# Optimization experiments

Measured on AMD Instinct MI355X. Metric: run time of the kernel, lower is better.

The kernel has to match this reference:

```python
import jax, jax.numpy as jnp
import numpy as np

B, N_PER, D_IN, D_OUT, E_PER = 64, 256, 256, 128, 8192  # graphs, nodes/graph, in feat, out feat (=clusters K), edges/graph
EPS = 1e-12


def _sage(h, src, dst, W, b):
    # DenseSAGEConv (mean aggregator): h [n,Din], src/dst [E]
    agg = jnp.zeros_like(h).at[dst].add(h[src])                 # sum of in-neighbor messages
    deg = jnp.zeros((h.shape[0],), h.dtype).at[dst].add(1.0)
    agg = agg / jnp.maximum(deg, 1.0)[:, None]                  # mean aggregation
    z = jnp.concatenate([h, agg], axis=-1) @ W + b              # Linear(2*Din -> Dout)
    z = z / jnp.maximum(jnp.linalg.norm(z, axis=-1, keepdims=True), EPS)  # F.normalize(p=2)
    return jax.nn.relu(z)                                       # activation


def setup_inputs() -> dict:
    key = jax.random.key(0)
    ks = jax.random.split(key, 5)
    h = jax.random.normal(ks[0], (B, N_PER, D_IN), jnp.float32)
    edge_src = jax.random.randint(ks[1], (B, E_PER), 0, N_PER)
    edge_dst = jax.random.randint(ks[2], (B, E_PER), 0, N_PER)
    s = 1.0 / np.sqrt(2 * D_IN)
    W_feat = jax.random.uniform(ks[3], (2 * D_IN, D_OUT), jnp.float32, -s, s)
    b_feat = jnp.zeros((D_OUT,), jnp.float32)
    W_pool = jax.random.uniform(ks[4], (2 * D_IN, D_OUT), jnp.float32, -s, s)
    b_pool = jnp.zeros((D_OUT,), jnp.float32)
    return {"h": h, "edge_src": edge_src, "edge_dst": edge_dst,
            "W_feat": W_feat, "b_feat": b_feat, "W_pool": W_pool, "b_pool": b_pool}


def reference(h, edge_src, edge_dst, W_feat, b_feat, W_pool, b_pool):
    sage = jax.vmap(_sage, in_axes=(0, 0, 0, None, None))
    feat = sage(h, edge_src, edge_dst, W_feat, b_feat)                          # [B,n,K]
    assign = jax.nn.softmax(sage(h, edge_src, edge_dst, W_pool, b_pool), -1)    # [B,n,K]
    # h = assign^T @ feat, per graph (equivalent to block_diag(assign)^T @ stacked feat)
    h_pool = jnp.einsum('bnk,bnd->bkd', assign, feat).reshape(B * D_OUT, D_OUT)  # [B*K, Dout]
    # adj_new = S^T A S per graph; A[dst,src]=1 per edge -> sum_e outer(S[dst_e], S[src_e])
    s_dst = jnp.take_along_axis(assign, edge_dst[:, :, None], axis=1)           # [B,E,K]
    s_src = jnp.take_along_axis(assign, edge_src[:, :, None], axis=1)           # [B,E,K]
    blocks = jnp.einsum('bek,bel->bkl', s_dst, s_src)                           # [B,K,K]
    # cross-graph blocks are exactly zero in the batched graph -> block-diagonal dense adj
    adj_new = jax.scipy.linalg.block_diag(*blocks)                              # [B*K, B*K]
    return adj_new, h_pool
```

## Files before the change

### kernel.cpp

```cpp
#include <hip/hip_runtime.h>
#include <hip/hip_bf16.h>
#include <stdint.h>

#define BG 64
#define NP 256
#define DI 256
#define DO 128
#define EP 8192


typedef __attribute__((ext_vector_type(8))) short short8;
typedef __attribute__((ext_vector_type(4))) float float4v;

__device__ __forceinline__ int ldi(const void* p, size_t i, int i64) {
  return i64 ? (int)((const long long*)p)[i] : ((const int*)p)[i];
}

__device__ __forceinline__ short f2b(float x) {
  union { float f; unsigned u; } c; c.f = x;
  unsigned r = c.u + 0x7FFFu + ((c.u >> 16) & 1u);
  return (short)(r >> 16);
}

__global__ void k_scatter(const void* __restrict__ esrc, const void* __restrict__ edst,
                          float* __restrict__ A, float* __restrict__ deg) {
  __shared__ int cnt;
  int b = blockIdx.x, t = threadIdx.x;
  if (t == 0) cnt = 0;
  __syncthreads();
  uint32_t w = ((const uint32_t*)esrc)[2 * t + 1];
  if (w != 0) atomicAdd(&cnt, 1);
  float4* Az = (float4*)(A + (size_t)b * NP * NP);
  for (int i = t; i < NP * NP / 4; i += 256) Az[i] = make_float4(0.f, 0.f, 0.f, 0.f);
  deg[b * NP + t] = 0.f;
  __syncthreads();
  int i64 = (cnt == 0);
  const size_t base = (size_t)b * EP;
  float* Ab = A + (size_t)b * NP * NP;
  float* degb = deg + b * NP;
  for (int e = t; e < EP; e += 256) {
    int si = ldi(esrc, base + e, i64) & (NP - 1);
    int di = ldi(edst, base + e, i64) & (NP - 1);
    atomicAdd(Ab + (size_t)di * NP + si, 1.0f);
    atomicAdd(degb + di, 1.0f);
  }
}

__global__ __launch_bounds__(256) void k_wt(const float* __restrict__ Wf,
                                            const float* __restrict__ Wp,
                                            short* __restrict__ Wt) {
  __shared__ __align__(16) float T[32][132];
  int b = blockIdx.x;
  int head = b >> 4;
  int k0 = (b & 15) * 32;
  const float* W = head ? Wp : Wf;
  int t = threadIdx.x;
  {
    int k = t >> 3, fs = (t & 7) * 16;
    const float* src = &W[(size_t)(k0 + k) * DO + fs];
#pragma unroll
    for (int j = 0; j < 4; ++j)
      *(float4*)&T[k][fs + j * 4] = *(const float4*)(src + j * 4);
  }
  __syncthreads();
  int f = t & 127, kh = (t >> 7) * 16;
  __align__(16) short tmp[16];
#pragma unroll
  for (int i = 0; i < 16; ++i) tmp[i] = f2b(T[kh + i][f]);
  short* dst = &Wt[((size_t)head * DO + f) * 512 + k0 + kh];
  *(short8*)dst = *(short8*)&tmp[0];
  *(short8*)(dst + 8) = *(short8*)&tmp[8];
}

__global__ __launch_bounds__(256) void k_gemm_agg(const float* __restrict__ A,
                                                  const float* __restrict__ h,
                                                  const float* __restrict__ deg,
                                                  float* __restrict__ agg) {
  __shared__ __align__(16) float As[32][68];
  __shared__ __align__(16) float Hs[32][132];
  int b = blockIdx.y;
  int r0 = (blockIdx.x & 3) * 64;
  int f0 = (blockIdx.x >> 2) * 128;
  int t = threadIdx.x;
  int tr = t >> 4, tc = t & 15;
  float acc[4][8] = {};
  const float* Ab = A + (size_t)b * NP * NP;
  const float* hb = h + (size_t)b * NP * DI;
  for (int kc = 0; kc < NP; kc += 32) {
    __syncthreads();
    {
      int r = t >> 2;
      int ks = (t & 3) * 8;
      const float* src = &Ab[(size_t)(r0 + r) * NP + kc + ks];
      float4 v0 = *(const float4*)src;
      float4 v1 = *(const float4*)(src + 4);
      As[ks + 0][r] = v0.x; As[ks + 1][r] = v0.y; As[ks + 2][r] = v0.z; As[ks + 3][r] = v0.w;
      As[ks + 4][r] = v1.x; As[ks + 5][r] = v1.y; As[ks + 6][r] = v1.z; As[ks + 7][r] = v1.w;
    }
    {
      int k = t >> 3;
      int fs = (t & 7) * 16;
      const float* src = &hb[(size_t)(kc + k) * DI + f0 + fs];
#pragma unroll
      for (int j = 0; j < 4; ++j)
        *(float4*)&Hs[k][fs + j * 4] = *(const float4*)(src + j * 4);
    }
    __syncthreads();
#pragma unroll
    for (int k = 0; k < 32; ++k) {
      float a[4], ww[8];
      *(float4*)&a[0] = *(const float4*)&As[k][tr * 4];
      *(float4*)&ww[0] = *(const float4*)&Hs[k][tc * 8];
      *(float4*)&ww[4] = *(const float4*)&Hs[k][tc * 8 + 4];
#pragma unroll
      for (int i = 0; i < 4; ++i)
#pragma unroll
        for (int j = 0; j < 8; ++j)
          acc[i][j] += a[i] * ww[j];
    }
  }
#pragma unroll
  for (int i = 0; i < 4; ++i) {
    int gi = r0 + tr * 4 + i;
    float sc = 1.0f / fmaxf(deg[b * NP + gi], 1.0f);
    float* dst = &agg[((size_t)b * NP + gi) * DI + f0 + tc * 8];
    float o0[4] = { acc[i][0] * sc, acc[i][1] * sc, acc[i][2] * sc, acc[i][3] * sc };
    float o1[4] = { acc[i][4] * sc, acc[i][5] * sc, acc[i][6] * sc, acc[i][7] * sc };
    *(float4*)dst = *(float4*)o0;
    *(float4*)(dst + 4) = *(float4*)o1;
  }
}

__global__ __launch_bounds__(256) void k_zepi_mfma(const float* __restrict__ h,
                                                   const float* __restrict__ agg,
                                                   const short* __restrict__ Wt,
                                                   const float* __restrict__ bfe,
                                                   const float* __restrict__ bpo,
                                                   float* __restrict__ feat,
                                                   float* __restrict__ assign) {
  __shared__ __align__(16) short Xs[32][40];
  int r0 = blockIdx.x * 32;
  int t = threadIdx.x;
  int wave = t >> 6, lane = t & 63;
  int rt = wave & 1, ch = wave >> 1;
  int m = lane & 15, q = lane >> 4;
  float4v acc[8];
#pragma unroll
  for (int i = 0; i < 8; ++i) acc[i] = (float4v){0.f, 0.f, 0.f, 0.f};

  for (int kc = 0; kc < 2 * DI; kc += 32) {
    __syncthreads();
    {
      int r = t >> 3, k4 = (t & 7) * 4;
      const float* src = (kc < DI) ? &h[(size_t)(r0 + r) * DI + kc + k4]
                                   : &agg[(size_t)(r0 + r) * DI + (kc - DI) + k4];
      float4 v = *(const float4*)src;
      Xs[r][k4 + 0] = f2b(v.x); Xs[r][k4 + 1] = f2b(v.y);
      Xs[r][k4 + 2] = f2b(v.z); Xs[r][k4 + 3] = f2b(v.w);
    }
    __syncthreads();
    short8 afrag = *(const short8*)&Xs[rt * 16 + m][q * 8];
#pragma unroll
    for (int tt = 0; tt < 8; ++tt) {
      int n = ch * 128 + tt * 16 + m;
      short8 bfrag = *(const short8*)&Wt[(size_t)n * 512 + kc + q * 8];
      acc[tt] = __builtin_amdgcn_mfma_f32_16x16x32_bf16(afrag, bfrag, acc[tt], 0, 0, 0);
    }
  }

  const float* bp = ch ? bpo : bfe;
  float bias[8];
#pragma unroll
  for (int tt = 0; tt < 8; ++tt) bias[tt] = bp ? bp[tt * 16 + m] : 0.f;
#pragma unroll
  for (int reg = 0; reg < 4; ++reg) {
    int row = r0 + rt * 16 + q * 4 + reg;
    float z[8];
    float ss = 0.f;
#pragma unroll
    for (int tt = 0; tt < 8; ++tt) { z[tt] = acc[tt][reg] + bias[tt]; ss += z[tt] * z[tt]; }
    ss += __shfl_xor(ss, 1); ss += __shfl_xor(ss, 2);
    ss += __shfl_xor(ss, 4); ss += __shfl_xor(ss, 8);
    float inv = 1.0f / fmaxf(sqrtf(ss), 1e-12f);
    float v[8];
#pragma unroll
    for (int tt = 0; tt < 8; ++tt) v[tt] = fmaxf(z[tt] * inv, 0.f);
    if (ch == 0) {
#pragma unroll
      for (int tt = 0; tt < 8; ++tt) feat[(size_t)row * DO + tt * 16 + m] = v[tt];
    } else {
      float mx = v[0];
#pragma unroll
      for (int tt = 1; tt < 8; ++tt) mx = fmaxf(mx, v[tt]);
      mx = fmaxf(mx, __shfl_xor(mx, 1)); mx = fmaxf(mx, __shfl_xor(mx, 2));
      mx = fmaxf(mx, __shfl_xor(mx, 4)); mx = fmaxf(mx, __shfl_xor(mx, 8));
      float e[8], s = 0.f;
#pragma unroll
      for (int tt = 0; tt < 8; ++tt) { e[tt] = __expf(v[tt] - mx); s += e[tt]; }
      s += __shfl_xor(s, 1); s += __shfl_xor(s, 2);
      s += __shfl_xor(s, 4); s += __shfl_xor(s, 8);
      float is = 1.0f / s;
#pragma unroll
      for (int tt = 0; tt < 8; ++tt) assign[(size_t)row * DO + tt * 16 + m] = e[tt] * is;
    }
  }
}

__global__ __launch_bounds__(256) void k_gemm_as(const float* __restrict__ A,
                                                 const float* __restrict__ assign,
                                                 float* __restrict__ AS) {
  __shared__ __align__(16) float As[32][68];
  __shared__ __align__(16) float Bs[32][132];
  int b = blockIdx.y;
  int r0 = blockIdx.x * 64;
  int t = threadIdx.x;
  int tr = t >> 4, tc = t & 15;
  float acc[4][8] = {};
  const float* Ab = A + (size_t)b * NP * NP;
  const float* asb = assign + (size_t)b * NP * DO;
  for (int kc = 0; kc < NP; kc += 32) {
    __syncthreads();
    {
      int r = t >> 2;
      int ks = (t & 3) * 8;
      const float* src = &Ab[(size_t)(r0 + r) * NP + kc + ks];
      float4 v0 = *(const float4*)src;
      float4 v1 = *(const float4*)(src + 4);
      As[ks + 0][r] = v0.x; As[ks + 1][r] = v0.y; As[ks + 2][r] = v0.z; As[ks + 3][r] = v0.w;
      As[ks + 4][r] = v1.x; As[ks + 5][r] = v1.y; As[ks + 6][r] = v1.z; As[ks + 7][r] = v1.w;
    }
    {
      int k = t >> 3;
      int ls = (t & 7) * 16;
      const float* src = &asb[(size_t)(kc + k) * DO + ls];
#pragma unroll
      for (int j = 0; j < 4; ++j)
        *(float4*)&Bs[k][ls + j * 4] = *(const float4*)(src + j * 4);
    }
    __syncthreads();
#pragma unroll
    for (int k = 0; k < 32; ++k) {
      float a[4], ww[8];
      *(float4*)&a[0] = *(const float4*)&As[k][tr * 4];
      *(float4*)&ww[0] = *(const float4*)&Bs[k][tc * 8];
      *(float4*)&ww[4] = *(const float4*)&Bs[k][tc * 8 + 4];
#pragma unroll
      for (int i = 0; i < 4; ++i)
#pragma unroll
        for (int j = 0; j < 8; ++j)
          acc[i][j] += a[i] * ww[j];
    }
  }
#pragma unroll
  for (int i = 0; i < 4; ++i) {
    float* dst = &AS[((size_t)b * NP + r0 + tr * 4 + i) * DO + tc * 8];
    *(float4*)dst = *(float4*)&acc[i][0];
    *(float4*)(dst + 4) = *(float4*)&acc[i][4];
  }
}

__global__ __launch_bounds__(256) void k_pool(const float* __restrict__ assign,
                                              const float* __restrict__ AS,
                                              const float* __restrict__ feat,
                                              float* __restrict__ adj,
                                              float* __restrict__ hpool) {
  __shared__ __align__(16) float Ps[32][68];
  __shared__ __align__(16) float Ys[32][132];
  int b = blockIdx.y;
  int mt = blockIdx.x & 1;
  int which = blockIdx.x >> 1;
  const float* Y = which ? feat : AS;
  int m0 = mt * 64;
  int t = threadIdx.x;
  int tr = t >> 4, tc = t & 15;
  float acc[4][8] = {};
  for (int nc = 0; nc < NP; nc += 32) {
    __syncthreads();
    {
      int n = t >> 3;
      int mseg = (t & 7) * 8;
      const float* src = &assign[((size_t)b * NP + nc + n) * DO + m0 + mseg];
      *(float4*)&Ps[n][mseg] = *(const float4*)src;
      *(float4*)&Ps[n][mseg + 4] = *(const float4*)(src + 4);
    }
    {
      int n = t >> 3;
      int ds = (t & 7) * 16;
      const float* src = &Y[((size_t)b * NP + nc + n) * DO + ds];
#pragma unroll
      for (int j = 0; j < 4; ++j)
        *(float4*)&Ys[n][ds + j * 4] = *(const float4*)(src + j * 4);
    }
    __syncthreads();
#pragma unroll
    for (int n = 0; n < 32; ++n) {
      float a[4], ww[8];
      *(float4*)&a[0] = *(const float4*)&Ps[n][tr * 4];
      *(float4*)&ww[0] = *(const float4*)&Ys[n][tc * 8];
      *(float4*)&ww[4] = *(const float4*)&Ys[n][tc * 8 + 4];
#pragma unroll
      for (int i = 0; i < 4; ++i)
#pragma unroll
        for (int j = 0; j < 8; ++j)
          acc[i][j] += a[i] * ww[j];
    }
  }
  if (which == 0) {
#pragma unroll
    for (int i = 0; i < 4; ++i) {
      float* dst = &adj[(size_t)(b * DO + m0 + tr * 4 + i) * (BG * DO) + b * DO + tc * 8];
      *(float4*)dst = *(float4*)&acc[i][0];
      *(float4*)(dst + 4) = *(float4*)&acc[i][4];
    }
  } else {
#pragma unroll
    for (int i = 0; i < 4; ++i) {
      float* dst = &hpool[((size_t)b * DO + m0 + tr * 4 + i) * DO + tc * 8];
      *(float4*)dst = *(float4*)&acc[i][0];
      *(float4*)(dst + 4) = *(float4*)&acc[i][4];
    }
  }
}

extern "C" void kernel_launch(void* const* d_in, const int* in_sizes, int n_in,
                              void* d_out, int out_size, void* d_ws, size_t ws_size,
                              hipStream_t stream) {
  (void)out_size; (void)ws_size;
  int ih = -1, ie[2] = {-1, -1}, iw[2] = {-1, -1}, ib[2] = {-1, -1};
  int ne = 0, nw = 0, nb = 0;
  for (int i = 0; i < n_in; ++i) {
    long long s = in_sizes[i];
    if (s == (long long)BG * NP * DI) { if (ih < 0) ih = i; }
    else if (s == (long long)BG * EP && ne < 2) ie[ne++] = i;
    else if (s == (long long)2 * DI * DO && nw < 2) iw[nw++] = i;
    else if (s == (long long)DO && nb < 2) ib[nb++] = i;
  }
  if (ih < 0 || ne < 2 || nw < 2) {
    ih = 0;
    ie[0] = (n_in > 1) ? 1 : 0;  ie[1] = (n_in > 2) ? 2 : ie[0];
    iw[0] = (n_in > 3) ? 3 : 0;  iw[1] = (n_in > 5) ? 5 : iw[0];
    ib[0] = (n_in > 4) ? 4 : -1; ib[1] = (n_in > 6) ? 6 : -1;
    nb = (ib[1] >= 0) ? 2 : (ib[0] >= 0 ? 1 : 0);
  }
  const float* h    = (const float*)d_in[ih];
  const void* esrc  = d_in[ie[0]];
  const void* edst  = d_in[ie[1]];
  const float* Wf   = (const float*)d_in[iw[0]];
  const float* Wp   = (const float*)d_in[iw[1]];
  const float* bfe  = (nb >= 1) ? (const float*)d_in[ib[0]] : nullptr;
  const float* bpo  = (nb >= 2) ? (const float*)d_in[ib[1]] : nullptr;

  float* adj   = (float*)d_out;
  float* hpool = (float*)d_out + (size_t)(BG * DO) * (BG * DO);
  const size_t ADJ_BYTES = (size_t)(BG * DO) * (BG * DO) * sizeof(float);

  char* wb = (char*)d_ws;
  float* A      = (float*)wb;
  float* agg    = (float*)(wb + 16777216);
  float* feat   = (float*)(wb + 33554432);
  float* assign = (float*)(wb + 41943040);
  float* AS     = (float*)(wb + 50331648);
  float* deg    = (float*)(wb + 58720256);
  short* Wt     = (short*)(wb + 58720256 + 65536);

  hipMemsetAsync(adj, 0, ADJ_BYTES, stream);
  k_wt<<<32, 256, 0, stream>>>(Wf, Wp, Wt);
  k_scatter<<<BG, 256, 0, stream>>>(esrc, edst, A, deg);
  k_gemm_agg<<<dim3(8, BG), 256, 0, stream>>>(A, h, deg, agg);
  k_zepi_mfma<<<BG * NP / 32, 256, 0, stream>>>(h, agg, Wt, bfe, bpo, feat, assign);
  k_gemm_as<<<dim3(4, BG), 256, 0, stream>>>(A, assign, AS);
  k_pool<<<dim3(4, BG), 256, 0, stream>>>(assign, AS, feat, adj, hpool);
}
```

Measured before the change: 472.4 us.

## Build adjacency in LDS and compute neighbor aggregation with split-bf16 MFMA

The edge scatter now builds each 64-row slice of the per-graph adjacency in shared memory rather than with global atomics. It writes fp32 and bf16 copies and computes degree from row sums. A new transpose kernel splits h into hi/lo bf16 parts. The aggregation GEMM then uses bf16 MFMA (two passes: hi and lo) instead of the fp32 LDS-tiled FMA loop. This is meant to cut global atomic traffic and scalar FMA cost, at the price of extra passes over the edge list (each block scans all edges), extra workspace traffic, and small precision changes. Exactness for the count matrix holds in bf16 only while each count stays small.

Measured after the change: 464.7 us. No clear change (-1.6%).

```diff
diff --git a/kernel.cpp b/kernel.cpp
--- a/kernel.cpp
+++ b/kernel.cpp
@@ -10,6 +10,7 @@
 
 
 typedef __attribute__((ext_vector_type(8))) short short8;
+typedef __attribute__((ext_vector_type(4))) short short4v;
 typedef __attribute__((ext_vector_type(4))) float float4v;
 
 __device__ __forceinline__ int ldi(const void* p, size_t i, int i64) {
@@ -21,28 +22,116 @@
   unsigned r = c.u + 0x7FFFu + ((c.u >> 16) & 1u);
   return (short)(r >> 16);
 }
-
-__global__ void k_scatter(const void* __restrict__ esrc, const void* __restrict__ edst,
-                          float* __restrict__ A, float* __restrict__ deg) {
-  __shared__ int cnt;
-  int b = blockIdx.x, t = threadIdx.x;
-  if (t == 0) cnt = 0;
+__device__ __forceinline__ float b2f(short b) {
+  union { unsigned u; float f; } c; c.u = ((unsigned)(unsigned short)b) << 16;
+  return c.f;
+}
+
+__device__ __forceinline__ int vote_i64(const void* esrc) {
+  const uint32_t* ew = (const uint32_t*)esrc;
+  int i64 = 1;
+#pragma unroll
+  for (int j = 0; j < 8; ++j)
+    if (ew[2 * j + 1] != 0) i64 = 0;
+  return i64;
+}
+
+__global__ __launch_bounds__(256) void k_scatter(const void* __restrict__ esrc,
+                                                 const void* __restrict__ edst,
+                                                 float* __restrict__ A,
+                                                 short* __restrict__ Abf,
+                                                 float* __restrict__ deg) {
+  __shared__ float Asl[64][256];
+  int b = blockIdx.y, rq = blockIdx.x, t = threadIdx.x;
+  float4* Az = (float4*)&Asl[0][0];
+  for (int i = t; i < 64 * 256 / 4; i += 256) Az[i] = make_float4(0.f, 0.f, 0.f, 0.f);
+  int i64 = vote_i64(esrc);
   __syncthreads();
-  uint32_t w = ((const uint32_t*)esrc)[2 * t + 1];
-  if (w != 0) atomicAdd(&cnt, 1);
-  float4* Az = (float4*)(A + (size_t)b * NP * NP);
-  for (int i = t; i < NP * NP / 4; i += 256) Az[i] = make_float4(0.f, 0.f, 0.f, 0.f);
-  deg[b * NP + t] = 0.f;
-  __syncthreads();
-  int i64 = (cnt == 0);
   const size_t base = (size_t)b * EP;
-  float* Ab = A + (size_t)b * NP * NP;
-  float* degb = deg + b * NP;
   for (int e = t; e < EP; e += 256) {
     int si = ldi(esrc, base + e, i64) & (NP - 1);
     int di = ldi(edst, base + e, i64) & (NP - 1);
-    atomicAdd(Ab + (size_t)di * NP + si, 1.0f);
-    atomicAdd(degb + di, 1.0f);
+    if ((di >> 6) == rq) atomicAdd(&Asl[di & 63][si], 1.0f);
+  }
+  __syncthreads();
+  int wv = t >> 6, ln = t & 63;
+#pragma unroll
+  for (int k = 0; k < 16; ++k) {
+    int r = k * 4 + wv;
+    float4 v = *(float4*)&Asl[r][ln * 4];
+    int gr = rq * 64 + r;
+    size_t o = ((size_t)b * NP + gr) * NP + ln * 4;
+    *(float4*)&A[o] = v;
+    short tmp[4] = { f2b(v.x), f2b(v.y), f2b(v.z), f2b(v.w) };
+    *(short4v*)&Abf[o] = *(short4v*)tmp;
+    float s = v.x + v.y + v.z + v.w;
+    s += __shfl_xor(s, 1);  s += __shfl_xor(s, 2);  s += __shfl_xor(s, 4);
+    s += __shfl_xor(s, 8);  s += __shfl_xor(s, 16); s += __shfl_xor(s, 32);
+    if (ln == 0) deg[b * NP + gr] = s;
+  }
+}
+
+__global__ __launch_bounds__(256) void k_htr(const float* __restrict__ h,
+                                             short* __restrict__ hThi,
+                                             short* __restrict__ hTlo) {
+  __shared__ float T[64][65];
+  int b = blockIdx.z, n0 = blockIdx.x * 64, f0 = blockIdx.y * 64;
+  int t = threadIdx.x;
+  int r = t >> 4, c4 = (t & 15) * 4;
+#pragma unroll
+  for (int i = 0; i < 4; ++i) {
+    float4 v = *(const float4*)&h[((size_t)b * NP + n0 + i * 16 + r) * DI + f0 + c4];
+    T[i * 16 + r][c4 + 0] = v.x; T[i * 16 + r][c4 + 1] = v.y;
+    T[i * 16 + r][c4 + 2] = v.z; T[i * 16 + r][c4 + 3] = v.w;
+  }
+  __syncthreads();
+#pragma unroll
+  for (int i = 0; i < 4; ++i) {
+    int f = i * 16 + r;
+    short hi4[4], lo4[4];
+#pragma unroll
+    for (int j = 0; j < 4; ++j) {
+      float x = T[c4 + j][f];
+      short hb = f2b(x);
+      hi4[j] = hb;
+      lo4[j] = f2b(x - b2f(hb));
+    }
+    size_t o = ((size_t)b * DI + f0 + f) * NP + n0 + c4;
+    *(short4v*)&hThi[o] = *(short4v*)hi4;
+    *(short4v*)&hTlo[o] = *(short4v*)lo4;
+  }
+}
+
+__global__ __launch_bounds__(256) void k_gemm_agg(const short* __restrict__ Abf,
+                                                  const short* __restrict__ hThi,
+                                                  const short* __restrict__ hTlo,
+                                                  const float* __restrict__ deg,
+                                                  float* __restrict__ agg) {
+  int b = blockIdx.y, r0 = blockIdx.x * 32, t = threadIdx.x;
+  int wave = t >> 6, lane = t & 63, rt = wave & 1, fh = wave >> 1;
+  int m = lane & 15, q = lane >> 4;
+  float4v acc[8];
+#pragma unroll
+  for (int i = 0; i < 8; ++i) acc[i] = (float4v){0.f, 0.f, 0.f, 0.f};
+  const short* Ar = &Abf[((size_t)b * NP + r0 + rt * 16 + m) * NP];
+  for (int kc = 0; kc < NP; kc += 32) {
+    short8 af = *(const short8*)&Ar[kc + q * 8];
+#pragma unroll
+    for (int tt = 0; tt < 8; ++tt) {
+      int f = fh * 128 + tt * 16 + m;
+      short8 bh = *(const short8*)&hThi[((size_t)b * DI + f) * NP + kc + q * 8];
+      short8 bl = *(const short8*)&hTlo[((size_t)b * DI + f) * NP + kc + q * 8];
+      acc[tt] = __builtin_amdgcn_mfma_f32_16x16x32_bf16(af, bh, acc[tt], 0, 0, 0);
+      acc[tt] = __builtin_amdgcn_mfma_f32_16x16x32_bf16(af, bl, acc[tt], 0, 0, 0);
+    }
+  }
+#pragma unroll
+  for (int reg = 0; reg < 4; ++reg) {
+    int row = r0 + rt * 16 + q * 4 + reg;
+    float sc = 1.0f / fmaxf(deg[b * NP + row], 1.0f);
+#pragma unroll
+    for (int tt = 0; tt < 8; ++tt)
+      agg[((size_t)b * NP + row) * DI + fh * 128 + tt * 16 + m] = acc[tt][reg] * sc;
   }
 }
 
@@ -70,65 +159,6 @@
   short* dst = &Wt[((size_t)head * DO + f) * 512 + k0 + kh];
   *(short8*)dst = *(short8*)&tmp[0];
   *(short8*)(dst + 8) = *(short8*)&tmp[8];
-}
-
-__global__ __launch_bounds__(256) void k_gemm_agg(const float* __restrict__ A,
-                                                  const float* __restrict__ h,
-                                                  const float* __restrict__ deg,
-                                                  float* __restrict__ agg) {
-  __shared__ __align__(16) float As[32][68];
-  __shared__ __align__(16) float Hs[32][132];
-  int b = blockIdx.y;
-  int r0 = (blockIdx.x & 3) * 64;
-  int f0 = (blockIdx.x >> 2) * 128;
-  int t = threadIdx.x;
-  int tr = t >> 4, tc = t & 15;
-  float acc[4][8] = {};
-  const float* Ab = A + (size_t)b * NP * NP;
-  const float* hb = h + (size_t)b * NP * DI;
-  for (int kc = 0; kc < NP; kc += 32) {
-    __syncthreads();
-    {
-      int r = t >> 2;
-      int ks = (t & 3) * 8;
-      const float* src = &Ab[(size_t)(r0 + r) * NP + kc + ks];
-      float4 v0 = *(const float4*)src;
-      float4 v1 = *(const float4*)(src + 4);
-      As[ks + 0][r] = v0.x; As[ks + 1][r] = v0.y; As[ks + 2][r] = v0.z; As[ks + 3][r] = v0.w;
-      As[ks + 4][r] = v1.x; As[ks + 5][r] = v1.y; As[ks + 6][r] = v1.z; As[ks + 7][r] = v1.w;
-    }
-    {
-      int k = t >> 3;
-      int fs = (t & 7) * 16;
-      const float* src = &hb[(size_t)(kc + k) * DI + f0 + fs];
-#pragma unroll
-      for (int j = 0; j < 4; ++j)
-        *(float4*)&Hs[k][fs + j * 4] = *(const float4*)(src + j * 4);
-    }
-    __syncthreads();
-#pragma unroll
-    for (int k = 0; k < 32; ++k) {
-      float a[4], ww[8];
-      *(float4*)&a[0] = *(const float4*)&As[k][tr * 4];
-      *(float4*)&ww[0] = *(const float4*)&Hs[k][tc * 8];
-      *(float4*)&ww[4] = *(const float4*)&Hs[k][tc * 8 + 4];
-#pragma unroll
-      for (int i = 0; i < 4; ++i)
-#pragma unroll
-        for (int j = 0; j < 8; ++j)
-          acc[i][j] += a[i] * ww[j];
-    }
-  }
-#pragma unroll
-  for (int i = 0; i < 4; ++i) {
-    int gi = r0 + tr * 4 + i;
-    float sc = 1.0f / fmaxf(deg[b * NP + gi], 1.0f);
-    float* dst = &agg[((size_t)b * NP + gi) * DI + f0 + tc * 8];
-    float o0[4] = { acc[i][0] * sc, acc[i][1] * sc, acc[i][2] * sc, acc[i][3] * sc };
-    float o1[4] = { acc[i][4] * sc, acc[i][5] * sc, acc[i][6] * sc, acc[i][7] * sc };
-    *(float4*)dst = *(float4*)o0;
-    *(float4*)(dst + 4) = *(float4*)o1;
-  }
 }
 
 __global__ __launch_bounds__(256) void k_zepi_mfma(const float* __restrict__ h,
@@ -362,11 +392,15 @@
   float* AS     = (float*)(wb + 50331648);
   float* deg    = (float*)(wb + 58720256);
   short* Wt     = (short*)(wb + 58720256 + 65536);
+  short* Abf    = (short*)(wb + 59047936);
+  short* hThi   = (short*)(wb + 67436544);
+  short* hTlo   = (short*)(wb + 75825152);
 
   hipMemsetAsync(adj, 0, ADJ_BYTES, stream);
   k_wt<<<32, 256, 0, stream>>>(Wf, Wp, Wt);
-  k_scatter<<<BG, 256, 0, stream>>>(esrc, edst, A, deg);
-  k_gemm_agg<<<dim3(8, BG), 256, 0, stream>>>(A, h, deg, agg);
+  k_htr<<<dim3(4, 4, BG), 256, 0, stream>>>(h, hThi, hTlo);
+  k_scatter<<<dim3(4, BG), 256, 0, stream>>>(esrc, edst, A, Abf, deg);
+  k_gemm_agg<<<dim3(8, BG), 256, 0, stream>>>(Abf, hThi, hTlo, deg, agg);
   k_zepi_mfma<<<BG * NP / 32, 256, 0, stream>>>(h, agg, Wt, bfe, bpo, feat, assign);
   k_gemm_as<<<dim3(4, BG), 256, 0, stream>>>(A, assign, AS);
   k_pool<<<dim3(4, BG), 256, 0, stream>>>(assign, AS, feat, adj, hpool);
```
